# Performance work log

Measured on AMD Instinct MI355X. Metric: run time of the kernel, lower is better.

Reference implementation:

```python
import jax, jax.numpy as jnp
import numpy as np

N_NODES, N_EDGES = 100000, 400000
D_NODE, D_EDGE, N_COND, N_ROUNDS = 128, 64, 2, 3


def gru_cell(x, h, Wih, Whh, bih, bhh):
    # Standard torch.nn.GRUCell math. x: [N, D] input, h: [N, D] hidden.
    gi = x @ Wih.T + bih            # [N, 3D]
    gh = h @ Whh.T + bhh            # [N, 3D]
    ir, iz, inn = jnp.split(gi, 3, axis=-1)
    hr, hz, hn = jnp.split(gh, 3, axis=-1)
    r = jax.nn.sigmoid(ir + hr)
    z = jax.nn.sigmoid(iz + hz)
    n = jnp.tanh(inn + r * hn)
    return (1.0 - z) * n + z * h


def setup_inputs() -> dict:
    key = jax.random.key(0)
    ks = jax.random.split(key, 10)
    scale = jnp.float32(0.05)
    d_in = 2 * D_NODE + D_EDGE + N_COND  # 322, matches enc_U Linear in_features
    h = jax.random.normal(ks[0], (N_NODES, D_NODE), jnp.float32)
    e = jax.random.normal(ks[1], (N_EDGES, D_EDGE), jnp.float32)
    src = jax.random.randint(ks[2], (N_EDGES,), 0, N_NODES)
    dst = jax.random.randint(ks[3], (N_EDGES,), 0, N_NODES)
    cond = jax.random.normal(ks[4], (N_COND,), jnp.float32)
    U_W = jax.random.normal(ks[5], (N_ROUNDS, D_NODE, d_in), jnp.float32) * scale
    U_b = jnp.zeros((N_ROUNDS, D_NODE), jnp.float32)
    Wih = jax.random.normal(ks[6], (N_ROUNDS, 3 * D_NODE, D_NODE), jnp.float32) * scale
    Whh = jax.random.normal(ks[7], (N_ROUNDS, 3 * D_NODE, D_NODE), jnp.float32) * scale
    bih = jnp.zeros((N_ROUNDS, 3 * D_NODE), jnp.float32)
    bhh = jnp.zeros((N_ROUNDS, 3 * D_NODE), jnp.float32)
    return dict(h=h, e=e, src=src, dst=dst, cond=cond,
                U_W=U_W, U_b=U_b, Wih=Wih, Whh=Whh, bih=bih, bhh=bhh)


def reference(h, e, src, dst, cond, U_W, U_b, Wih, Whh, bih, bhh):
    # GGM encode(): 3 rounds of gather-concat-Linear(enc_U)-segment_sum-GRUCell(enc_C).
    n_nodes = h.shape[0]
    n_edges = e.shape[0]
    cond_e = jnp.broadcast_to(cond, (n_edges, cond.shape[0]))
    for k in range(U_W.shape[0]):
        # per-edge message input: [h_v, h_w, e_vw, condition] -> [E, 2D+DE+NC]
        x = jnp.concatenate([h[dst], h[src], e, cond_e], axis=-1)
        msg = x @ U_W[k].T + U_b[k]                              # [E, D]
        agg = jax.ops.segment_sum(msg, dst, num_segments=n_nodes)  # [N, D]
        h = gru_cell(agg, h, Wih[k], Whh[k], bih[k], bhh[k])
    return h
```

## Files before the change

### kernel.cpp

```cpp
#include <hip/hip_runtime.h>
#include <hip/hip_bf16.h>
#include <hip/hip_fp16.h>


#define D_NODE 128
#define D_EDGE 64
#define D_IN   322
#define GRU3   384
#define ROWS_BLK 128
#define PA_STRIDE 328
#define PB_STRIDE 136

typedef _Float16 f16x8 __attribute__((ext_vector_type(8)));
typedef _Float16 f16x4 __attribute__((ext_vector_type(4)));
typedef _Float16 f16x2 __attribute__((ext_vector_type(2)));
typedef float    f32x4 __attribute__((ext_vector_type(4)));
typedef unsigned short u16x8 __attribute__((ext_vector_type(8)));

__device__ __forceinline__ f16x8 as_f16x8(u16x8 v) { return __builtin_bit_cast(f16x8, v); }
__device__ __forceinline__ float sigm_(float x) { return 1.f / (1.f + __expf(-x)); }
__device__ __forceinline__ float tanh_(float x) { return 1.f - 2.f / (__expf(2.f * x) + 1.f); }

__global__ void hist_k(const int* __restrict__ dst, int* __restrict__ cnt, int E) {
    int t = blockIdx.x * 256 + threadIdx.x;
    if (t < E) atomicAdd(&cnt[dst[t]], 1);
}

__global__ __launch_bounds__(256) void scan1_k(const int* __restrict__ cnt, int* __restrict__ row_ptr,
                                               int* __restrict__ blk_sums, int N) {
    __shared__ int s[256];
    const int t = threadIdx.x;
    const int base = blockIdx.x * 1024 + t * 4;
    int v0 = (base + 0 < N) ? cnt[base + 0] : 0;
    int v1 = (base + 1 < N) ? cnt[base + 1] : 0;
    int v2 = (base + 2 < N) ? cnt[base + 2] : 0;
    int v3 = (base + 3 < N) ? cnt[base + 3] : 0;
    const int tot = v0 + v1 + v2 + v3;
    s[t] = tot;
    __syncthreads();
    for (int off = 1; off < 256; off <<= 1) {
        int u = (t >= off) ? s[t - off] : 0;
        __syncthreads();
        s[t] += u;
        __syncthreads();
    }
    const int excl = s[t] - tot;
    if (base + 0 < N) row_ptr[base + 0] = excl;
    if (base + 1 < N) row_ptr[base + 1] = excl + v0;
    if (base + 2 < N) row_ptr[base + 2] = excl + v0 + v1;
    if (base + 3 < N) row_ptr[base + 3] = excl + v0 + v1 + v2;
    if (t == 255) blk_sums[blockIdx.x] = s[255];
}

__global__ __launch_bounds__(256) void scan2_k(int* __restrict__ blk_sums, int NB,
                                               int* __restrict__ row_ptr, int N, int E) {
    __shared__ int s[256];
    const int t = threadIdx.x;
    const int v = (t < NB) ? blk_sums[t] : 0;
    s[t] = v;
    __syncthreads();
    for (int off = 1; off < 256; off <<= 1) {
        int u = (t >= off) ? s[t - off] : 0;
        __syncthreads();
        s[t] += u;
        __syncthreads();
    }
    if (t < NB) blk_sums[t] = s[t] - v;
    if (t == 0) row_ptr[N] = E;
}

__global__ __launch_bounds__(256) void scan3_k(int* __restrict__ row_ptr, int* __restrict__ cursor,
                                               const int* __restrict__ blk_sums, int N) {
    const int off = blk_sums[blockIdx.x];
    const int base = blockIdx.x * 1024 + threadIdx.x * 4;
#pragma unroll
    for (int j = 0; j < 4; ++j) {
        const int i = base + j;
        if (i < N) {
            const int v = row_ptr[i] + off;
            row_ptr[i] = v;
            cursor[i] = v;
        }
    }
}

__global__ void scatter_k(const int* __restrict__ src, const int* __restrict__ dst,
                          int* __restrict__ cursor, int* __restrict__ csr_src,
                          int* __restrict__ csr_eid, int E) {
    int t = blockIdx.x * 256 + threadIdx.x;
    if (t < E) {
        int d = dst[t];
        int pos = atomicAdd(&cursor[d], 1);
        csr_src[pos] = src[t];
        csr_eid[pos] = t;
    }
}

__global__ __launch_bounds__(320) void cvt_uwp_k(const float* __restrict__ in, _Float16* __restrict__ out) {
    const int row = blockIdx.x;
    const int t = threadIdx.x;
    out[(size_t)row * 320 + t] = (_Float16)in[(size_t)row * D_IN + t];
}

__global__ void cvt_f32_k(const float* __restrict__ in, _Float16* __restrict__ out, int n) {
    int t = blockIdx.x * 256 + threadIdx.x;
    if (t < n) out[t] = (_Float16)in[t];
}

__global__ void cvt4_k(const float* __restrict__ in, _Float16* __restrict__ out, int n4) {
    int t = blockIdx.x * 256 + threadIdx.x;
    if (t < n4) {
        const f32x4 v = ((const f32x4*)in)[t];
        f16x4 r;
        r[0] = (_Float16)v[0]; r[1] = (_Float16)v[1];
        r[2] = (_Float16)v[2]; r[3] = (_Float16)v[3];
        ((f16x4*)out)[t] = r;
    }
}

__global__ void cvt_out_k(const _Float16* __restrict__ in, float* __restrict__ out, int n4) {
    int t = blockIdx.x * 256 + threadIdx.x;
    if (t < n4) {
        const f16x4 v = ((const f16x4*)in)[t];
        f32x4 r;
        r[0] = (float)v[0]; r[1] = (float)v[1];
        r[2] = (float)v[2]; r[3] = (float)v[3];
        ((f32x4*)out)[t] = r;
    }
}

__global__ void compute_c_k(const float* __restrict__ UW, const float* __restrict__ Ub,
                            const float* __restrict__ cond, float* __restrict__ cvec) {
    int t = threadIdx.x;
    if (t < 3 * D_NODE) {
        int k = t >> 7, i = t & 127;
        const float* u = UW + (size_t)k * D_NODE * D_IN + (size_t)i * D_IN + 320;
        cvec[t] = u[0] * cond[0] + u[1] * cond[1] + Ub[k * D_NODE + i];
    }
}

__global__ __launch_bounds__(256) void gather_e_k(const float* __restrict__ e,
                                                  const int* __restrict__ row_ptr,
                                                  const int* __restrict__ csr_eid,
                                                  _Float16* __restrict__ S_e, int N) {
    const int wave = threadIdx.x >> 6, lane = threadIdx.x & 63;
    const int n = blockIdx.x * 4 + wave;
    if (n >= N) return;
    const int p0 = row_ptr[n], p1 = row_ptr[n + 1];
    float a = 0.f, b = 0.f, c = 0.f, d = 0.f;
    int p = p0;
    for (; p + 3 < p1; p += 4) {
        const int e0 = csr_eid[p], e1 = csr_eid[p + 1], e2 = csr_eid[p + 2], e3 = csr_eid[p + 3];
        a += e[(size_t)e0 * D_EDGE + lane];
        b += e[(size_t)e1 * D_EDGE + lane];
        c += e[(size_t)e2 * D_EDGE + lane];
        d += e[(size_t)e3 * D_EDGE + lane];
    }
    for (; p < p1; ++p) a += e[(size_t)csr_eid[p] * D_EDGE + lane];
    S_e[(size_t)n * D_EDGE + lane] = (_Float16)((a + b) + (c + d));
}

__global__ __launch_bounds__(256) void gather_e16_k(const _Float16* __restrict__ e16,
                                                    const int* __restrict__ row_ptr,
                                                    const int* __restrict__ csr_eid,
                                                    _Float16* __restrict__ S_e, int N) {
    const int wave = threadIdx.x >> 6, lane = threadIdx.x & 63;
    const int n = blockIdx.x * 4 + wave;
    if (n >= N) return;
    const int p0 = row_ptr[n], p1 = row_ptr[n + 1];
    float a = 0.f, b = 0.f, c = 0.f, d = 0.f;
    int p = p0;
    for (; p + 3 < p1; p += 4) {
        const int e0 = csr_eid[p], e1 = csr_eid[p + 1], e2 = csr_eid[p + 2], e3 = csr_eid[p + 3];
        a += (float)e16[(size_t)e0 * D_EDGE + lane];
        b += (float)e16[(size_t)e1 * D_EDGE + lane];
        c += (float)e16[(size_t)e2 * D_EDGE + lane];
        d += (float)e16[(size_t)e3 * D_EDGE + lane];
    }
    for (; p < p1; ++p) a += (float)e16[(size_t)csr_eid[p] * D_EDGE + lane];
    S_e[(size_t)n * D_EDGE + lane] = (_Float16)((a + b) + (c + d));
}

__global__ __launch_bounds__(256) void gather_h_k(const _Float16* __restrict__ h16,
                                                  const int* __restrict__ row_ptr,
                                                  const int* __restrict__ csr_src,
                                                  _Float16* __restrict__ S_h, int N) {
    const int wave = threadIdx.x >> 6, lane = threadIdx.x & 63;
    const int n = blockIdx.x * 4 + wave;
    if (n >= N) return;
    const unsigned* hp = (const unsigned*)h16;
    const int p0 = row_ptr[n], p1 = row_ptr[n + 1];
    float a0 = 0.f, a1 = 0.f, b0 = 0.f, b1 = 0.f;
    float c0 = 0.f, c1 = 0.f, d0 = 0.f, d1 = 0.f;
    int p = p0;
    for (; p + 3 < p1; p += 4) {
        const int s0 = csr_src[p], s1 = csr_src[p + 1], s2 = csr_src[p + 2], s3 = csr_src[p + 3];
        const f16x2 v0 = __builtin_bit_cast(f16x2, hp[(size_t)s0 * 64 + lane]);
        const f16x2 v1 = __builtin_bit_cast(f16x2, hp[(size_t)s1 * 64 + lane]);
        const f16x2 v2 = __builtin_bit_cast(f16x2, hp[(size_t)s2 * 64 + lane]);
        const f16x2 v3 = __builtin_bit_cast(f16x2, hp[(size_t)s3 * 64 + lane]);
        a0 += (float)v0[0]; a1 += (float)v0[1];
        b0 += (float)v1[0]; b1 += (float)v1[1];
        c0 += (float)v2[0]; c1 += (float)v2[1];
        d0 += (float)v3[0]; d1 += (float)v3[1];
    }
    for (; p < p1; ++p) {
        const f16x2 v = __builtin_bit_cast(f16x2, hp[(size_t)csr_src[p] * 64 + lane]);
        a0 += (float)v[0]; a1 += (float)v[1];
    }
    f16x2 r;
    r[0] = (_Float16)((a0 + b0) + (c0 + d0));
    r[1] = (_Float16)((a1 + b1) + (c1 + d1));
    ((unsigned*)S_h)[(size_t)n * 64 + lane] = __builtin_bit_cast(unsigned, r);
}

__global__ __launch_bounds__(256) void agg_k(
    const _Float16* __restrict__ h16,
    const _Float16* __restrict__ S_h,
    const _Float16* __restrict__ S_e,
    const int* __restrict__ row_ptr,
    const float* __restrict__ cvec,
    const _Float16* __restrict__ UWp,
    _Float16* __restrict__ agg,
    int N) {
    __shared__ __align__(16) _Float16 pbuf[2][16 * PA_STRIDE];

    const int tid  = threadIdx.x;
    const int wave = tid >> 6;
    const int lane = tid & 63;
    const int l15  = lane & 15;
    const int lg   = lane >> 4;
    const int rbase = blockIdx.x * ROWS_BLK + wave * 32;

    const unsigned short* hp  = (const unsigned short*)h16;
    const unsigned short* shp = (const unsigned short*)S_h;
    const unsigned short* sep = (const unsigned short*)S_e;
    const unsigned short* uwp = (const unsigned short*)UWp;

    f16x8 a_h[2][4], a_sh[2][4], a_se[2][2];
#pragma unroll
    for (int m = 0; m < 2; ++m) {
        const int arow = min(rbase + m * 16 + l15, N - 1);
#pragma unroll
        for (int kb = 0; kb < 4; ++kb) {
            a_h[m][kb]  = as_f16x8(*(const u16x8*)(hp  + (size_t)arow * D_NODE + kb * 32 + lg * 8));
            a_sh[m][kb] = as_f16x8(*(const u16x8*)(shp + (size_t)arow * D_NODE + kb * 32 + lg * 8));
        }
#pragma unroll
        for (int kb = 0; kb < 2; ++kb)
            a_se[m][kb] = as_f16x8(*(const u16x8*)(sep + (size_t)arow * D_EDGE + kb * 32 + lg * 8));
    }
    float degv[2][4];
#pragma unroll
    for (int m = 0; m < 2; ++m)
#pragma unroll
        for (int i = 0; i < 4; ++i) {
            const int n = min(rbase + m * 16 + lg * 4 + i, N - 1);
            degv[m][i] = (float)(row_ptr[n + 1] - row_ptr[n]);
        }

    u16x8 pr0, pr1, pr2;
    auto load_panel = [&](int nb) {
        const int c0 = tid, c1 = 256 + tid, c2 = 512 + tid;
        pr0 = *(const u16x8*)(uwp + (size_t)(nb * 16 + c0 / 40) * 320 + (c0 % 40) * 8);
        pr1 = *(const u16x8*)(uwp + (size_t)(nb * 16 + c1 / 40) * 320 + (c1 % 40) * 8);
        if (c2 < 640)
            pr2 = *(const u16x8*)(uwp + (size_t)(nb * 16 + c2 / 40) * 320 + (c2 % 40) * 8);
    };
    auto write_panel = [&](int b) {
        const int c0 = tid, c1 = 256 + tid, c2 = 512 + tid;
        *(u16x8*)&pbuf[b][(c0 / 40) * PA_STRIDE + (c0 % 40) * 8] = pr0;
        *(u16x8*)&pbuf[b][(c1 / 40) * PA_STRIDE + (c1 % 40) * 8] = pr1;
        if (c2 < 640)
            *(u16x8*)&pbuf[b][(c2 / 40) * PA_STRIDE + (c2 % 40) * 8] = pr2;
    };

    load_panel(0);
    write_panel(0);
    __syncthreads();

#pragma unroll 1
    for (int nb = 0; nb < 8; ++nb) {
        if (nb < 7) load_panel(nb + 1);
        const _Float16* bp = pbuf[nb & 1];
        f32x4 acc1[2] = {{0.f,0.f,0.f,0.f},{0.f,0.f,0.f,0.f}};
        f32x4 acc2[2] = {{0.f,0.f,0.f,0.f},{0.f,0.f,0.f,0.f}};
#pragma unroll
        for (int kb = 0; kb < 10; ++kb) {
            f16x8 b = as_f16x8(*(const u16x8*)&bp[l15 * PA_STRIDE + kb * 32 + lg * 8]);
            if (kb < 4) {
                acc1[0] = __builtin_amdgcn_mfma_f32_16x16x32_f16(a_h[0][kb], b, acc1[0], 0, 0, 0);
                acc1[1] = __builtin_amdgcn_mfma_f32_16x16x32_f16(a_h[1][kb], b, acc1[1], 0, 0, 0);
            } else if (kb < 8) {
                acc2[0] = __builtin_amdgcn_mfma_f32_16x16x32_f16(a_sh[0][kb-4], b, acc2[0], 0, 0, 0);
                acc2[1] = __builtin_amdgcn_mfma_f32_16x16x32_f16(a_sh[1][kb-4], b, acc2[1], 0, 0, 0);
            } else {
                acc2[0] = __builtin_amdgcn_mfma_f32_16x16x32_f16(a_se[0][kb-8], b, acc2[0], 0, 0, 0);
                acc2[1] = __builtin_amdgcn_mfma_f32_16x16x32_f16(a_se[1][kb-8], b, acc2[1], 0, 0, 0);
            }
        }
        const float cv = cvec[nb * 16 + l15];
#pragma unroll
        for (int m = 0; m < 2; ++m)
#pragma unroll
            for (int i = 0; i < 4; ++i) {
                const int n = rbase + m * 16 + lg * 4 + i;
                if (n < N)
                    agg[(size_t)n * D_NODE + nb * 16 + l15] =
                        (_Float16)(degv[m][i] * (acc1[m][i] + cv) + acc2[m][i]);
            }
        if (nb < 7) write_panel((nb + 1) & 1);
        __syncthreads();
    }
}

__global__ __launch_bounds__(256, 4) void gru_k(
    _Float16* __restrict__ h16,
    const _Float16* __restrict__ agg,
    const _Float16* __restrict__ Wihh,
    const _Float16* __restrict__ Whhh,
    const float* __restrict__ bih,
    const float* __restrict__ bhh,
    int N) {
    __shared__ __align__(16) _Float16 pbuf[2][96 * PB_STRIDE];

    const int tid  = threadIdx.x;
    const int wave = tid >> 6;
    const int lane = tid & 63;
    const int l15  = lane & 15;
    const int lg   = lane >> 4;
    const int rbase = blockIdx.x * ROWS_BLK + wave * 32;

    const unsigned short* hp  = (const unsigned short*)h16;
    const unsigned short* agp = (const unsigned short*)agg;
    const unsigned short* wih = (const unsigned short*)Wihh;
    const unsigned short* whh = (const unsigned short*)Whhh;

    f16x8 a_ag[2][4], a_h[2][4];
#pragma unroll
    for (int m = 0; m < 2; ++m) {
        const int arow = min(rbase + m * 16 + l15, N - 1);
#pragma unroll
        for (int kb = 0; kb < 4; ++kb) {
            a_ag[m][kb] = as_f16x8(*(const u16x8*)(agp + (size_t)arow * D_NODE + kb * 32 + lg * 8));
            a_h[m][kb]  = as_f16x8(*(const u16x8*)(hp  + (size_t)arow * D_NODE + kb * 32 + lg * 8));
        }
    }

    u16x8 pr[6];
    auto load_panel = [&](int nb) {
#pragma unroll
        for (int r = 0; r < 6; ++r) {
            const int c = r * 256 + tid;
            const int row = c >> 4;
            const int off = (c & 15) * 8;
            const int gate = row >> 4;
            const int col = nb * 16 + (row & 15) + (gate % 3) * D_NODE;
            const unsigned short* mat = (gate < 3) ? wih : whh;
            pr[r] = *(const u16x8*)(mat + (size_t)col * D_NODE + off);
        }
    };
    auto write_panel = [&](int b) {
#pragma unroll
        for (int r = 0; r < 6; ++r) {
            const int c = r * 256 + tid;
            const int row = c >> 4;
            const int off = (c & 15) * 8;
            *(u16x8*)&pbuf[b][row * PB_STRIDE + off] = pr[r];
        }
    };

    load_panel(0);
    write_panel(0);
    __syncthreads();

#pragma unroll 1
    for (int nb = 0; nb < 8; ++nb) {
        if (nb < 7) load_panel(nb + 1);
        const int d = nb * 16 + l15;
        float hv[2][4];
#pragma unroll
        for (int m = 0; m < 2; ++m)
#pragma unroll
            for (int i = 0; i < 4; ++i) {
                const int n = min(rbase + m * 16 + lg * 4 + i, N - 1);
                hv[m][i] = (float)h16[(size_t)n * D_NODE + d];
            }
        const float bir = bih[d],       biz = bih[128 + d], bin = bih[256 + d];
        const float bhr = bhh[d],       bhz = bhh[128 + d], bhn = bhh[256 + d];

        const _Float16* bp = pbuf[nb & 1];
        f32x4 air[2] = {{0.f,0.f,0.f,0.f},{0.f,0.f,0.f,0.f}};
        f32x4 aiz[2] = {{0.f,0.f,0.f,0.f},{0.f,0.f,0.f,0.f}};
        f32x4 ain_[2] = {{0.f,0.f,0.f,0.f},{0.f,0.f,0.f,0.f}};
        f32x4 ahr[2] = {{0.f,0.f,0.f,0.f},{0.f,0.f,0.f,0.f}};
        f32x4 ahz[2] = {{0.f,0.f,0.f,0.f},{0.f,0.f,0.f,0.f}};
        f32x4 ahn[2] = {{0.f,0.f,0.f,0.f},{0.f,0.f,0.f,0.f}};
#pragma unroll
        for (int kb = 0; kb < 4; ++kb) {
            const int ko = kb * 32 + lg * 8;
            f16x8 b;
            b = as_f16x8(*(const u16x8*)&bp[(0 * 16 + l15) * PB_STRIDE + ko]);
            air[0] = __builtin_amdgcn_mfma_f32_16x16x32_f16(a_ag[0][kb], b, air[0], 0, 0, 0);
            air[1] = __builtin_amdgcn_mfma_f32_16x16x32_f16(a_ag[1][kb], b, air[1], 0, 0, 0);
            b = as_f16x8(*(const u16x8*)&bp[(1 * 16 + l15) * PB_STRIDE + ko]);
            aiz[0] = __builtin_amdgcn_mfma_f32_16x16x32_f16(a_ag[0][kb], b, aiz[0], 0, 0, 0);
            aiz[1] = __builtin_amdgcn_mfma_f32_16x16x32_f16(a_ag[1][kb], b, aiz[1], 0, 0, 0);
            b = as_f16x8(*(const u16x8*)&bp[(2 * 16 + l15) * PB_STRIDE + ko]);
            ain_[0] = __builtin_amdgcn_mfma_f32_16x16x32_f16(a_ag[0][kb], b, ain_[0], 0, 0, 0);
            ain_[1] = __builtin_amdgcn_mfma_f32_16x16x32_f16(a_ag[1][kb], b, ain_[1], 0, 0, 0);
            b = as_f16x8(*(const u16x8*)&bp[(3 * 16 + l15) * PB_STRIDE + ko]);
            ahr[0] = __builtin_amdgcn_mfma_f32_16x16x32_f16(a_h[0][kb], b, ahr[0], 0, 0, 0);
            ahr[1] = __builtin_amdgcn_mfma_f32_16x16x32_f16(a_h[1][kb], b, ahr[1], 0, 0, 0);
            b = as_f16x8(*(const u16x8*)&bp[(4 * 16 + l15) * PB_STRIDE + ko]);
            ahz[0] = __builtin_amdgcn_mfma_f32_16x16x32_f16(a_h[0][kb], b, ahz[0], 0, 0, 0);
            ahz[1] = __builtin_amdgcn_mfma_f32_16x16x32_f16(a_h[1][kb], b, ahz[1], 0, 0, 0);
            b = as_f16x8(*(const u16x8*)&bp[(5 * 16 + l15) * PB_STRIDE + ko]);
            ahn[0] = __builtin_amdgcn_mfma_f32_16x16x32_f16(a_h[0][kb], b, ahn[0], 0, 0, 0);
            ahn[1] = __builtin_amdgcn_mfma_f32_16x16x32_f16(a_h[1][kb], b, ahn[1], 0, 0, 0);
        }
#pragma unroll
        for (int m = 0; m < 2; ++m)
#pragma unroll
            for (int i = 0; i < 4; ++i) {
                const int n = rbase + m * 16 + lg * 4 + i;
                if (n < N) {
                    const float r  = sigm_(air[m][i] + bir + ahr[m][i] + bhr);
                    const float z  = sigm_(aiz[m][i] + biz + ahz[m][i] + bhz);
                    const float nn = tanh_(ain_[m][i] + bin + r * (ahn[m][i] + bhn));
                    h16[(size_t)n * D_NODE + d] = (_Float16)((1.f - z) * nn + z * hv[m][i]);
                }
            }
        if (nb < 7) write_panel((nb + 1) & 1);
        __syncthreads();
    }
}

extern "C" void kernel_launch(void* const* d_in, const int* in_sizes, int n_in,
                              void* d_out, int out_size, void* d_ws, size_t ws_size,
                              hipStream_t stream) {
    const float* h0   = (const float*)d_in[0];
    const float* e    = (const float*)d_in[1];
    const int*   src  = (const int*)d_in[2];
    const int*   dst  = (const int*)d_in[3];
    const float* cond = (const float*)d_in[4];
    const float* UW   = (const float*)d_in[5];
    const float* Ub   = (const float*)d_in[6];
    const float* Wih  = (const float*)d_in[7];
    const float* Whh  = (const float*)d_in[8];
    const float* bih  = (const float*)d_in[9];
    const float* bhh  = (const float*)d_in[10];

    const int N = in_sizes[0] / D_NODE;
    const int E = in_sizes[2];
    const int NB = (N + 1023) / 1024;
    const int NT = (N + ROWS_BLK - 1) / ROWS_BLK;

    char* wsb = (char*)d_ws;
    size_t off = 0;
    auto carve = [&](size_t bytes) -> char* {
        char* p = wsb + off;
        off = (off + bytes + 255) & ~(size_t)255;
        return p;
    };
    int*   cnt      = (int*)carve((size_t)N * 4);
    int*   row_ptr  = (int*)carve(((size_t)N + 1) * 4);
    int*   cursor   = (int*)carve((size_t)N * 4);
    int*   csr_src  = (int*)carve((size_t)E * 4);
    int*   csr_eid  = (int*)carve((size_t)E * 4);
    int*   blk_sums = (int*)carve(256 * 4);
    float* cvec     = (float*)carve(3 * D_NODE * 4);
    _Float16* S_e  = (_Float16*)carve((size_t)N * D_EDGE * 2);
    _Float16* S_h  = (_Float16*)carve((size_t)N * D_NODE * 2);
    _Float16* aggb = (_Float16*)carve((size_t)N * D_NODE * 2);
    _Float16* h16  = (_Float16*)carve((size_t)N * D_NODE * 2);
    _Float16* UWp  = (_Float16*)carve((size_t)3 * D_NODE * 320 * 2);
    _Float16* Wihh = (_Float16*)carve((size_t)3 * GRU3 * D_NODE * 2);
    _Float16* Whhh = (_Float16*)carve((size_t)3 * GRU3 * D_NODE * 2);
    const size_t e16_bytes = (size_t)E * D_EDGE * 2;
    _Float16* e16 = nullptr;
    if (off + e16_bytes + 256 <= ws_size) e16 = (_Float16*)carve(e16_bytes);
    (void)n_in; (void)out_size;

    hipMemsetAsync(cnt, 0, (size_t)N * 4, stream);
    hist_k<<<(E + 255) / 256, 256, 0, stream>>>(dst, cnt, E);
    scan1_k<<<NB, 256, 0, stream>>>(cnt, row_ptr, blk_sums, N);
    scan2_k<<<1, 256, 0, stream>>>(blk_sums, NB, row_ptr, N, E);
    scan3_k<<<NB, 256, 0, stream>>>(row_ptr, cursor, blk_sums, N);
    scatter_k<<<(E + 255) / 256, 256, 0, stream>>>(src, dst, cursor, csr_src, csr_eid, E);
    compute_c_k<<<1, 384, 0, stream>>>(UW, Ub, cond, cvec);
    cvt_uwp_k<<<3 * D_NODE, 320, 0, stream>>>(UW, UWp);
    {
        const int n1 = 3 * GRU3 * D_NODE;
        cvt_f32_k<<<(n1 + 255) / 256, 256, 0, stream>>>(Wih, Wihh, n1);
        cvt_f32_k<<<(n1 + 255) / 256, 256, 0, stream>>>(Whh, Whhh, n1);
    }
    {
        const int n4 = N * D_NODE / 4;
        cvt4_k<<<(n4 + 255) / 256, 256, 0, stream>>>(h0, h16, n4);
    }
    if (e16) {
        const int n4 = E * D_EDGE / 4;
        cvt4_k<<<(n4 + 255) / 256, 256, 0, stream>>>(e, e16, n4);
        gather_e16_k<<<(N + 3) / 4, 256, 0, stream>>>(e16, row_ptr, csr_eid, S_e, N);
    } else {
        gather_e_k<<<(N + 3) / 4, 256, 0, stream>>>(e, row_ptr, csr_eid, S_e, N);
    }

    for (int k = 0; k < 3; ++k) {
        gather_h_k<<<(N + 3) / 4, 256, 0, stream>>>(h16, row_ptr, csr_src, S_h, N);
        agg_k<<<NT, 256, 0, stream>>>(
            h16, S_h, S_e, row_ptr, cvec + k * D_NODE,
            UWp + (size_t)k * D_NODE * 320, aggb, N);
        gru_k<<<NT, 256, 0, stream>>>(
            h16, aggb,
            Wihh + (size_t)k * GRU3 * D_NODE,
            Whhh + (size_t)k * GRU3 * D_NODE,
            bih + (size_t)k * GRU3,
            bhh + (size_t)k * GRU3,
            N);
    }
    {
        const int n4 = N * D_NODE / 4;
        cvt_out_k<<<(n4 + 255) / 256, 256, 0, stream>>>(h16, (float*)d_out, n4);
    }
}
```

Measured before the change: 565.6 us.

## Widen gather loads to half-wave per node and double GEMM block size

The gather kernels now give each node half a wavefront, and each lane loads wider vectors: 4 halves for h and 2 halves for e, where before a full wave did narrower loads. This doubles the number of nodes per block and raises bytes per load instruction. The agg and GRU kernels move to 512 threads and 256 rows per block, so each weight panel staged in shared memory is shared by twice as many rows. In exchange there are fewer blocks, per-block occupancy limits may tighten, and the launch bounds of (512,4) may limit registers.

```diff
diff --git a/kernel.cpp b/kernel.cpp
--- a/kernel.cpp
+++ b/kernel.cpp
@@ -7,7 +7,7 @@
 #define D_EDGE 64
 #define D_IN   322
 #define GRU3   384
-#define ROWS_BLK 128
+#define ROWS_BLK 256
 #define PA_STRIDE 328
 #define PB_STRIDE 136
 
@@ -165,20 +165,33 @@
                                                     const int* __restrict__ csr_eid,
                                                     _Float16* __restrict__ S_e, int N) {
     const int wave = threadIdx.x >> 6, lane = threadIdx.x & 63;
-    const int n = blockIdx.x * 4 + wave;
+    const int half = lane >> 5, ln = lane & 31;
+    const int n = blockIdx.x * 8 + wave * 2 + half;
     if (n >= N) return;
+    const unsigned* ep = (const unsigned*)e16;
     const int p0 = row_ptr[n], p1 = row_ptr[n + 1];
-    float a = 0.f, b = 0.f, c = 0.f, d = 0.f;
+    float a0 = 0.f, a1 = 0.f, b0 = 0.f, b1 = 0.f;
+    float c0 = 0.f, c1 = 0.f, d0 = 0.f, d1 = 0.f;
     int p = p0;
     for (; p + 3 < p1; p += 4) {
         const int e0 = csr_eid[p], e1 = csr_eid[p + 1], e2 = csr_eid[p + 2], e3 = csr_eid[p + 3];
-        a += (float)e16[(size_t)e0 * D_EDGE + lane];
-        b += (float)e16[(size_t)e1 * D_EDGE + lane];
-        c += (float)e16[(size_t)e2 * D_EDGE + lane];
-        d += (float)e16[(size_t)e3 * D_EDGE + lane];
-    }
-    for (; p < p1; ++p) a += (float)e16[(size_t)csr_eid[p] * D_EDGE + lane];
-    S_e[(size_t)n * D_EDGE + lane] = (_Float16)((a + b) + (c + d));
+        const f16x2 v0 = __builtin_bit_cast(f16x2, ep[(size_t)e0 * 32 + ln]);
+        const f16x2 v1 = __builtin_bit_cast(f16x2, ep[(size_t)e1 * 32 + ln]);
+        const f16x2 v2 = __builtin_bit_cast(f16x2, ep[(size_t)e2 * 32 + ln]);
+        const f16x2 v3 = __builtin_bit_cast(f16x2, ep[(size_t)e3 * 32 + ln]);
+        a0 += (float)v0[0]; a1 += (float)v0[1];
+        b0 += (float)v1[0]; b1 += (float)v1[1];
+        c0 += (float)v2[0]; c1 += (float)v2[1];
+        d0 += (float)v3[0]; d1 += (float)v3[1];
+    }
+    for (; p < p1; ++p) {
+        const f16x2 v = __builtin_bit_cast(f16x2, ep[(size_t)csr_eid[p] * 32 + ln]);
+        a0 += (float)v[0]; a1 += (float)v[1];
+    }
+    f16x2 r;
+    r[0] = (_Float16)((a0 + b0) + (c0 + d0));
+    r[1] = (_Float16)((a1 + b1) + (c1 + d1));
+    ((unsigned*)S_e)[(size_t)n * 32 + ln] = __builtin_bit_cast(unsigned, r);
 }
 
 __global__ __launch_bounds__(256) void gather_h_k(const _Float16* __restrict__ h16,
@@ -186,35 +199,38 @@
                                                   const int* __restrict__ csr_src,
                                                   _Float16* __restrict__ S_h, int N) {
     const int wave = threadIdx.x >> 6, lane = threadIdx.x & 63;
-    const int n = blockIdx.x * 4 + wave;
+    const int half = lane >> 5, ln = lane & 31;
+    const int n = blockIdx.x * 8 + wave * 2 + half;
     if (n >= N) return;
-    const unsigned* hp = (const unsigned*)h16;
+    const uint2* hp = (const uint2*)h16;
     const int p0 = row_ptr[n], p1 = row_ptr[n + 1];
-    float a0 = 0.f, a1 = 0.f, b0 = 0.f, b1 = 0.f;
-    float c0 = 0.f, c1 = 0.f, d0 = 0.f, d1 = 0.f;
+    float aA[4] = {0.f,0.f,0.f,0.f}, aB[4] = {0.f,0.f,0.f,0.f};
+    float aC[4] = {0.f,0.f,0.f,0.f}, aD[4] = {0.f,0.f,0.f,0.f};
     int p = p0;
     for (; p + 3 < p1; p += 4) {
         const int s0 = csr_src[p], s1 = csr_src[p + 1], s2 = csr_src[p + 2], s3 = csr_src[p + 3];
-        const f16x2 v0 = __builtin_bit_cast(f16x2, hp[(size_t)s0 * 64 + lane]);
-        const f16x2 v1 = __builtin_bit_cast(f16x2, hp[(size_t)s1 * 64 + lane]);
-        const f16x2 v2 = __builtin_bit_cast(f16x2, hp[(size_t)s2 * 64 + lane]);
-        const f16x2 v3 = __builtin_bit_cast(f16x2, hp[(size_t)s3 * 64 + lane]);
-        a0 += (float)v0[0]; a1 += (float)v0[1];
-        b0 += (float)v1[0]; b1 += (float)v1[1];
-        c0 += (float)v2[0]; c1 += (float)v2[1];
-        d0 += (float)v3[0]; d1 += (float)v3[1];
+        const f16x4 v0 = __builtin_bit_cast(f16x4, hp[(size_t)s0 * 32 + ln]);
+        const f16x4 v1 = __builtin_bit_cast(f16x4, hp[(size_t)s1 * 32 + ln]);
+        const f16x4 v2 = __builtin_bit_cast(f16x4, hp[(size_t)s2 * 32 + ln]);
+        const f16x4 v3 = __builtin_bit_cast(f16x4, hp[(size_t)s3 * 32 + ln]);
+#pragma unroll
+        for (int j = 0; j < 4; ++j) {
+            aA[j] += (float)v0[j]; aB[j] += (float)v1[j];
+            aC[j] += (float)v2[j]; aD[j] += (float)v3[j];
+        }
     }
     for (; p < p1; ++p) {
-        const f16x2 v = __builtin_bit_cast(f16x2, hp[(size_t)csr_src[p] * 64 + lane]);
-        a0 += (float)v[0]; a1 += (float)v[1];
-    }
-    f16x2 r;
-    r[0] = (_Float16)((a0 + b0) + (c0 + d0));
-    r[1] = (_Float16)((a1 + b1) + (c1 + d1));
-    ((unsigned*)S_h)[(size_t)n * 64 + lane] = __builtin_bit_cast(unsigned, r);
-}
-
-__global__ __launch_bounds__(256) void agg_k(
+        const f16x4 v = __builtin_bit_cast(f16x4, hp[(size_t)csr_src[p] * 32 + ln]);
+#pragma unroll
+        for (int j = 0; j < 4; ++j) aA[j] += (float)v[j];
+    }
+    f16x4 r;
+#pragma unroll
+    for (int j = 0; j < 4; ++j) r[j] = (_Float16)((aA[j] + aB[j]) + (aC[j] + aD[j]));
+    ((uint2*)S_h)[(size_t)n * 32 + ln] = __builtin_bit_cast(uint2, r);
+}
+
+__global__ __launch_bounds__(512, 4) void agg_k(
     const _Float16* __restrict__ h16,
     const _Float16* __restrict__ S_h,
     const _Float16* __restrict__ S_e,
@@ -259,20 +275,18 @@
             degv[m][i] = (float)(row_ptr[n + 1] - row_ptr[n]);
         }
 
-    u16x8 pr0, pr1, pr2;
+    u16x8 pr0, pr1;
     auto load_panel = [&](int nb) {
-        const int c0 = tid, c1 = 256 + tid, c2 = 512 + tid;
+        const int c0 = tid, c1 = 512 + tid;
         pr0 = *(const u16x8*)(uwp + (size_t)(nb * 16 + c0 / 40) * 320 + (c0 % 40) * 8);
-        pr1 = *(const u16x8*)(uwp + (size_t)(nb * 16 + c1 / 40) * 320 + (c1 % 40) * 8);
-        if (c2 < 640)
-            pr2 = *(const u16x8*)(uwp + (size_t)(nb * 16 + c2 / 40) * 320 + (c2 % 40) * 8);
+        if (c1 < 640)
+            pr1 = *(const u16x8*)(uwp + (size_t)(nb * 16 + c1 / 40) * 320 + (c1 % 40) * 8);
     };
     auto write_panel = [&](int b) {
-        const int c0 = tid, c1 = 256 + tid, c2 = 512 + tid;
+        const int c0 = tid, c1 = 512 + tid;
         *(u16x8*)&pbuf[b][(c0 / 40) * PA_STRIDE + (c0 % 40) * 8] = pr0;
-        *(u16x8*)&pbuf[b][(c1 / 40) * PA_STRIDE + (c1 % 40) * 8] = pr1;
-        if (c2 < 640)
-            *(u16x8*)&pbuf[b][(c2 / 40) * PA_STRIDE + (c2 % 40) * 8] = pr2;
+        if (c1 < 640)
+            *(u16x8*)&pbuf[b][(c1 / 40) * PA_STRIDE + (c1 % 40) * 8] = pr1;
     };
 
     load_panel(0);
@@ -314,7 +328,7 @@
     }
 }
 
-__global__ __launch_bounds__(256, 4) void gru_k(
+__global__ __launch_bounds__(512, 4) void gru_k(
     _Float16* __restrict__ h16,
     const _Float16* __restrict__ agg,
     const _Float16* __restrict__ Wihh,
@@ -347,11 +361,11 @@
         }
     }
 
-    u16x8 pr[6];
+    u16x8 pr[3];
     auto load_panel = [&](int nb) {
 #pragma unroll
-        for (int r = 0; r < 6; ++r) {
-            const int c = r * 256 + tid;
+        for (int r = 0; r < 3; ++r) {
+            const int c = r * 512 + tid;
             const int row = c >> 4;
             const int off = (c & 15) * 8;
             const int gate = row >> 4;
@@ -362,8 +376,8 @@
     };
     auto write_panel = [&](int b) {
 #pragma unroll
-        for (int r = 0; r < 6; ++r) {
-            const int c = r * 256 + tid;
+        for (int r = 0; r < 3; ++r) {
+            const int c = r * 512 + tid;
             const int row = c >> 4;
             const int off = (c & 15) * 8;
             *(u16x8*)&pbuf[b][row * PB_STRIDE + off] = pr[r];
@@ -502,17 +516,17 @@
     if (e16) {
         const int n4 = E * D_EDGE / 4;
         cvt4_k<<<(n4 + 255) / 256, 256, 0, stream>>>(e, e16, n4);
-        gather_e16_k<<<(N + 3) / 4, 256, 0, stream>>>(e16, row_ptr, csr_eid, S_e, N);
+        gather_e16_k<<<(N + 7) / 8, 256, 0, stream>>>(e16, row_ptr, csr_eid, S_e, N);
     } else {
         gather_e_k<<<(N + 3) / 4, 256, 0, stream>>>(e, row_ptr, csr_eid, S_e, N);
     }
 
     for (int k = 0; k < 3; ++k) {
-        gather_h_k<<<(N + 3) / 4, 256, 0, stream>>>(h16, row_ptr, csr_src, S_h, N);
-        agg_k<<<NT, 256, 0, stream>>>(
+        gather_h_k<<<(N + 7) / 8, 256, 0, stream>>>(h16, row_ptr, csr_src, S_h, N);
+        agg_k<<<NT, 512, 0, stream>>>(
             h16, S_h, S_e, row_ptr, cvec + k * D_NODE,
             UWp + (size_t)k * D_NODE * 320, aggb, N);
-        gru_k<<<NT, 256, 0, stream>>>(
+        gru_k<<<NT, 512, 0, stream>>>(
             h16, aggb,
             Wihh + (size_t)k * GRU3 * D_NODE,
             Whhh + (size_t)k * GRU3 * D_NODE,
```

Measured after the change: 741.5 us. 1.31x slower.
